# Kernel tuning notes

Hardware: AMD Instinct MI355X
Metric: run time of the kernel (lower is better)

Reference implementation:

```python
import jax, jax.numpy as jnp
import numpy as np

D, H, F, Z = 768, 12, 2048, 100   # d_model, nhead, dim_feedforward, d_z
NL = 2                            # num enc layers == num dec layers
RATIO = 0.05                      # filter_ratio
EPS = 1e-5


def _ln(x, g, b):
    m = x.mean(-1, keepdims=True)
    v = ((x - m) ** 2).mean(-1, keepdims=True)
    return (x - m) / jnp.sqrt(v + EPS) * g + b


def _mha(x, bias, qkv_w, qkv_b, out_w, out_b):
    # x: [N, L, D] (torch seq-first: seq=N responses, batch=L token positions)
    # bias: [L, N] float key-padding mask, ADDED to logits (torch float-mask semantics)
    N, L, _ = x.shape
    hd = D // H
    qkv = jnp.einsum('nld,ed->nle', x, qkv_w) + qkv_b
    q, k, v = jnp.split(qkv, 3, axis=-1)
    q = q.reshape(N, L, H, hd)
    k = k.reshape(N, L, H, hd)
    v = v.reshape(N, L, H, hd)
    scores = jnp.einsum('nlhd,mlhd->lhnm', q, k) / jnp.sqrt(jnp.float32(hd))
    scores = scores + bias[:, None, None, :]
    attn = jax.nn.softmax(scores, axis=-1)
    o = jnp.einsum('lhnm,mlhd->nlhd', attn, v).reshape(N, L, D)
    return o @ out_w.T + out_b


def _stack(x, bias, p):
    qkv_w, qkv_b, out_w, out_b, g1, b1, w1, c1, w2, c2, g2, b2 = p
    for i in range(NL):  # post-norm TransformerEncoderLayer, relu FFN, eval (no dropout)
        a = _mha(x, bias, qkv_w[i], qkv_b[i], out_w[i], out_b[i])
        x = _ln(x + a, g1[i], b1[i])
        f = jax.nn.relu(x @ w1[i].T + c1[i]) @ w2[i].T + c2[i]
        x = _ln(x + f, g2[i], b2[i])
    return x


def _anomaly_scores(emb, msk, enc_p, dec_p, pe_w, pe_b, pd_w, pd_b):
    bias = msk.T  # [L, N]
    h = _stack(emb, bias, enc_p)
    z = jnp.tanh(h @ pe_w.T + pe_b)
    zd = jnp.tanh(z @ pd_w.T + pd_b)
    d = _stack(zd, bias, dec_p)
    # per-response MSE between mean decoded and mean input embedding, summed over D
    return ((d.mean(axis=1) - emb.mean(axis=1)) ** 2).sum(-1)


def _forward(tree_lens, inputs_embeds, attention_mask, enc_p, dec_p, pe_w, pe_b, pd_w, pd_b):
    B, T, L, _ = inputs_embeds.shape
    tls = np.asarray(tree_lens)
    n_resp = tls - 1
    # pack ragged replies: rows 1..tree_len-1 of every tree -> [Ntot, L, D]
    b_idx = np.concatenate([np.full(n, b) for b, n in enumerate(n_resp)])
    t_idx = np.concatenate([np.arange(1, tl) for tl in tls])
    reply = inputs_embeds[b_idx, t_idx]
    masks = attention_mask[b_idx, t_idx]
    s = _anomaly_scores(reply, masks, enc_p, dec_p, pe_w, pe_b, pd_w, pd_b)  # [Ntot]
    Ntot = s.shape[0]
    # original: rank_idx = global_argsort filtered to indices < n_resp[b] (min is always 0)
    # == argsort of the FIRST n_resp[b] packed scores (faithful to the source's indexing)
    masked = jnp.where(jnp.arange(Ntot)[None, :] < jnp.asarray(n_resp)[:, None],
                       s[None, :], jnp.inf)
    order = jnp.argsort(masked, axis=1)[:, :T - 1]  # [B, T-1]
    n_ext = np.maximum(np.floor(n_resp * RATIO).astype(np.int64), 1)
    sel = np.arange(T - 1)[None, :] < n_ext[:, None]          # [B, T-1]
    selj = jnp.asarray(sel)
    node_idx = jnp.where(selj, order + 1, 0)                  # pad slots reuse src (node 0)
    node_full = jnp.concatenate([jnp.zeros((B, 1), node_idx.dtype), node_idx], axis=1)
    brow = jnp.arange(B)[:, None]
    new_emb = inputs_embeds[brow, node_full]                  # [B, T, L, D]
    valid = jnp.asarray(np.concatenate([np.ones((B, 1), bool), sel], axis=1)
                        ).astype(attention_mask.dtype)
    new_msk = attention_mask[brow, node_full] * valid[:, :, None]  # pad rows get zero mask
    ohidx = jnp.where(selj, order + 1, T)                     # dump masked scatters to col T
    oh = jnp.zeros((B, T + 1), jnp.int32).at[brow, ohidx].set(1)[:, :T].at[:, 0].set(1)
    ext_mask = jnp.repeat(oh[:, :, None], L, axis=2).reshape(B, T * L)
    new_tree_lens = jnp.asarray(1 + n_ext, dtype=jnp.int32)
    n_ext_adv = 0
    return oh, ext_mask, n_ext_adv, new_tree_lens, new_emb, new_msk


def setup_inputs() -> dict:
    B, T, L = 16, 32, 64
    key = jax.random.key(0)
    ks = list(jax.random.split(key, 4))
    inp = {
        'tree_lens': jax.random.randint(ks[0], (B,), T // 2, T + 1),
        'inputs_embeds': jax.random.normal(ks[1], (B, T, L, D), jnp.float32),
        'attention_mask': jnp.ones((B, T, L), jnp.float32),
    }
    kit = iter(jax.random.split(ks[2], 32))
    def w(shape):
        return jax.random.normal(next(kit), (NL,) + shape, jnp.float32) * 0.02
    for pre in ('enc', 'dec'):
        inp[pre + '_qkv_w'] = w((3 * D, D)); inp[pre + '_qkv_b'] = jnp.zeros((NL, 3 * D))
        inp[pre + '_out_w'] = w((D, D));     inp[pre + '_out_b'] = jnp.zeros((NL, D))
        inp[pre + '_ln1_g'] = jnp.ones((NL, D)); inp[pre + '_ln1_b'] = jnp.zeros((NL, D))
        inp[pre + '_w1'] = w((F, D)); inp[pre + '_c1'] = jnp.zeros((NL, F))
        inp[pre + '_w2'] = w((D, F)); inp[pre + '_c2'] = jnp.zeros((NL, D))
        inp[pre + '_ln2_g'] = jnp.ones((NL, D)); inp[pre + '_ln2_b'] = jnp.zeros((NL, D))
    inp['pe_w'] = jax.random.normal(next(kit), (Z, D), jnp.float32) * 0.02
    inp['pe_b'] = jnp.zeros((Z,), jnp.float32)
    inp['pd_w'] = jax.random.normal(next(kit), (D, Z), jnp.float32) * 0.02
    inp['pd_b'] = jnp.zeros((D,), jnp.float32)
    return inp


def reference(tree_lens, inputs_embeds, attention_mask,
              enc_qkv_w, enc_qkv_b, enc_out_w, enc_out_b, enc_ln1_g, enc_ln1_b,
              enc_w1, enc_c1, enc_w2, enc_c2, enc_ln2_g, enc_ln2_b,
              dec_qkv_w, dec_qkv_b, dec_out_w, dec_out_b, dec_ln1_g, dec_ln1_b,
              dec_w1, dec_c1, dec_w2, dec_c2, dec_ln2_g, dec_ln2_b,
              pe_w, pe_b, pd_w, pd_b):
    enc_p = (enc_qkv_w, enc_qkv_b, enc_out_w, enc_out_b, enc_ln1_g, enc_ln1_b,
             enc_w1, enc_c1, enc_w2, enc_c2, enc_ln2_g, enc_ln2_b)
    dec_p = (dec_qkv_w, dec_qkv_b, dec_out_w, dec_out_b, dec_ln1_g, dec_ln1_b,
             dec_w1, dec_c1, dec_w2, dec_c2, dec_ln2_g, dec_ln2_b)
    return _forward(tree_lens, inputs_embeds, attention_mask, enc_p, dec_p,
                    pe_w, pe_b, pd_w, pd_b)
```

## Files before the change

kernel.cpp:

```cpp
#include <hip/hip_runtime.h>
#include <hip/hip_bf16.h>
#include <math.h>


#define B_  16
#define T_  32
#define L_  64
#define D_  768
#define H_  12
#define F_  2048
#define ZR_ 100
#define NP_ 512
#define EPS_ 1e-5f

#define MI_NTOT  0
#define MI_NRESP 8
#define MI_OFF   32
#define MI_BIDX  64
#define MI_TIDX  576
#define MI_NODE  1088

#define WS_BIAS2 2048
#define WS_EMEAN 34816
#define WS_S     428032
#define WS_WST   428544
#define WS_BIG   1313280

#define PEB_F    (WS_WST + 196608)

#define OUT_OH   0
#define OUT_EXT  512
#define OUT_NEA  33280
#define OUT_NTL  33281
#define OUT_NEMB 33297
#define OUT_NMSK 25199121
#define OUT_XSCR 33300
#define OUT_WSTK 12616224

#define WSEG0 1769472
#define WSEG1 589824
#define WSEG2 1572864
#define WSEG3 1572864
#define WPASS 5505024

typedef __attribute__((ext_vector_type(8))) short short8;
typedef __attribute__((ext_vector_type(4))) float f32x4;

__device__ inline float bf2f(unsigned s) {
  return __uint_as_float((s & 0xffffu) << 16);
}
__device__ inline unsigned short f2bf(float x) {
  unsigned u = __float_as_uint(x);
  u += 0x7fffu + ((u >> 16) & 1u);
  return (unsigned short)(u >> 16);
}
__device__ inline unsigned pack2(float a, float b) {
  return (unsigned)f2bf(a) | ((unsigned)f2bf(b) << 16);
}

__global__ void meta_kernel(const int* __restrict__ tl, int* __restrict__ mi) {
  if (threadIdx.x != 0) return;
  int off = 0;
  for (int b = 0; b < B_; b++) {
    int nr = tl[b] - 1;
    mi[MI_NRESP + b] = nr;
    mi[MI_OFF + b] = off;
    off += nr;
  }
  mi[MI_NTOT] = off;
  for (int j = 0; j < NP_; j++) {
    int b = -1, t = 0;
    if (j < off) {
      b = 0;
      while (b + 1 < B_ && j >= mi[MI_OFF + b + 1]) b++;
      t = j - mi[MI_OFF + b] + 1;
    }
    mi[MI_BIDX + j] = b;
    mi[MI_TIDX + j] = t;
  }
}

__global__ __launch_bounds__(256) void w2bf4_kernel(
    const float* __restrict__ s0, const float* __restrict__ s1,
    const float* __restrict__ s2, const float* __restrict__ s3,
    unsigned short* __restrict__ dst) {
  const int e = blockIdx.x * 1024 + threadIdx.x * 4;
  const float* src;
  int off;
  if (e < WSEG0)                         { src = s0; off = e; }
  else if (e < WSEG0 + WSEG1)            { src = s1; off = e - WSEG0; }
  else if (e < WSEG0 + WSEG1 + WSEG2)    { src = s2; off = e - WSEG0 - WSEG1; }
  else                                   { src = s3; off = e - WSEG0 - WSEG1 - WSEG2; }
  float4 v = *(const float4*)(src + off);
  uint2 pk; pk.x = pack2(v.x, v.y); pk.y = pack2(v.z, v.w);
  *(uint2*)(dst + e) = pk;
}

__global__ __launch_bounds__(256) void pepd_stage(
    const float* __restrict__ pew, const float* __restrict__ peb,
    const float* __restrict__ pdw,
    unsigned short* __restrict__ dpe, unsigned short* __restrict__ dpd,
    float* __restrict__ dpeb) {
  const int blk = blockIdx.x, t = threadIdx.x;
  if (blk < 192) {
    const int e = blk * 1024 + t * 4;
    const int r = e / 768, c = e % 768;
    float v[4];
    #pragma unroll
    for (int j = 0; j < 4; j++) v[j] = (r < ZR_) ? pew[r * 768 + c + j] : 0.f;
    uint2 pk; pk.x = pack2(v[0], v[1]); pk.y = pack2(v[2], v[3]);
    *(uint2*)(dpe + e) = pk;
  } else if (blk < 384) {
    const int e = (blk - 192) * 1024 + t * 4;
    const int r = e / 256, c = e % 256;
    float v[4];
    #pragma unroll
    for (int j = 0; j < 4; j++) v[j] = (c + j < ZR_) ? pdw[r * ZR_ + c + j] : 0.f;
    uint2 pk; pk.x = pack2(v[0], v[1]); pk.y = pack2(v[2], v[3]);
    *(uint2*)(dpd + e) = pk;
  } else {
    dpeb[t] = (t < ZR_) ? peb[t] : 0.f;
  }
}

__global__ __launch_bounds__(192) void gather_kernel(
    const float* __restrict__ emb, const float* __restrict__ am,
    const int* __restrict__ mi, unsigned short* __restrict__ X,
    float* __restrict__ bias2) {
  const int blk = blockIdx.x;
  const int j = blk >> 6, l = blk & 63;
  const int ntot = mi[MI_NTOT];
  const int t = threadIdx.x;
  float4 v = make_float4(0.f, 0.f, 0.f, 0.f);
  if (j < ntot) {
    const int b = mi[MI_BIDX + j], tt = mi[MI_TIDX + j];
    v = ((const float4*)(emb + (size_t)((b * T_ + tt) * L_ + l) * D_))[t];
    if (t == 0) bias2[blk] = am[(b * T_ + tt) * L_ + l];
  } else {
    if (t == 0) bias2[blk] = -1e30f;
  }
  uint2 pk; pk.x = pack2(v.x, v.y); pk.y = pack2(v.z, v.w);
  *(uint2*)(X + (size_t)blk * D_ + t * 4) = pk;
}

__global__ __launch_bounds__(256) void zerotail_kernel(const int* __restrict__ mi,
                                                       unsigned short* __restrict__ BIG) {
  const int row = blockIdx.x;
  if (row < mi[MI_NTOT] * 64) return;
  uint4 z = make_uint4(0u, 0u, 0u, 0u);
  uint4* p = (uint4*)(BIG + (size_t)row * 2304);
  for (int c = threadIdx.x; c < 288; c += 256) p[c] = z;
}

__global__ __launch_bounds__(256) void emean_kernel(const unsigned short* __restrict__ X,
                                                    float* __restrict__ em) {
  const int j = blockIdx.x;
  int d = threadIdx.x;
  for (int c = 0; c < 3; c++, d += 256) {
    const unsigned short* p = X + (size_t)j * L_ * D_ + d;
    float s = 0.f;
    for (int l = 0; l < L_; l++) s += bf2f(p[l * D_]);
    em[j * D_ + d] = s * (1.f / 64.f);
  }
}

__device__ inline float blockSum256(float v, float* red) {
  #pragma unroll
  for (int o = 32; o > 0; o >>= 1) v += __shfl_down(v, o);
  const int lane = threadIdx.x & 63, wid = threadIdx.x >> 6;
  __syncthreads();
  if (lane == 0) red[wid] = v;
  __syncthreads();
  return red[0] + red[1] + red[2] + red[3];
}

__global__ __launch_bounds__(256) void ln_kernel(unsigned short* __restrict__ X,
                                                 const float* __restrict__ g,
                                                 const float* __restrict__ bb,
                                                 const int* __restrict__ mi) {
  const int row = blockIdx.x;
  if (row >= mi[MI_NTOT] * L_) return;
  unsigned short* p = X + (size_t)row * D_;
  const int t = threadIdx.x;
  __shared__ float red[4];
  float v0 = bf2f(p[t]), v1 = bf2f(p[t + 256]), v2 = bf2f(p[t + 512]);
  float s = blockSum256(v0 + v1 + v2, red);
  float m = s * (1.f / 768.f);
  float d0 = v0 - m, d1 = v1 - m, d2 = v2 - m;
  float q = blockSum256(d0 * d0 + d1 * d1 + d2 * d2, red);
  float r = rsqrtf(q * (1.f / 768.f) + EPS_);
  p[t]       = f2bf(d0 * r * g[t]       + bb[t]);
  p[t + 256] = f2bf(d1 * r * g[t + 256] + bb[t + 256]);
  p[t + 512] = f2bf(d2 * r * g[t + 512] + bb[t + 512]);
}

template <int ACT, bool ADD>
__global__ __launch_bounds__(512, 2) void gemm_mfma(
    const unsigned short* __restrict__ A, int lda, int K,
    const unsigned short* __restrict__ W, int ldw,
    const float* __restrict__ bias,
    unsigned short* __restrict__ C, int ldc, int CT,
    const int* __restrict__ mi) {
  const int rows = mi[MI_NTOT] * 64;
  const int RTa = (rows + 255) >> 8;
  const int NTa = RTa * CT;
  const int id = blockIdx.x;
  if (id >= NTa) return;
  const int q8 = NTa >> 3, r8 = NTa & 7;
  const int xcd = id & 7, idx = id >> 3;
  const int wg = (xcd < r8 ? xcd * (q8 + 1) : r8 * (q8 + 1) + (xcd - r8) * q8) + idx;
  const int row0 = (wg / CT) * 256;
  const int col0 = (wg % CT) * 256;
  __shared__ unsigned short As[2][256 * 64];
  __shared__ unsigned short Bs[2][256 * 64];
  const int t = threadIdx.x;
  const int lane = t & 63, w = t >> 6;
  const int wr = w >> 2, wc = w & 3;
  const int quad = lane >> 4, l15 = lane & 15;

  const int srow = t >> 3;
  const int sgs = (t & 7) ^ (srow & 7);
  const unsigned short* aSrc = A + (size_t)(row0 + srow) * lda + sgs * 8;
  const unsigned short* bSrc = W + (size_t)(col0 + srow) * ldw + sgs * 8;

#define STAGE_(ph, kk, Ad, Bd)                                                  \
  do {                                                                          \
    __builtin_amdgcn_global_load_lds(                                           \
        (const __attribute__((address_space(1))) void*)(aSrc + (size_t)(ph) * 64 * lda + (kk)), \
        (__attribute__((address_space(3))) void*)((Ad) + (ph) * 4096 + w * 512), 16, 0, 0); \
    __builtin_amdgcn_global_load_lds(                                           \
        (const __attribute__((address_space(1))) void*)(bSrc + (size_t)(ph) * 64 * ldw + (kk)), \
        (__attribute__((address_space(3))) void*)((Bd) + (ph) * 4096 + w * 512), 16, 0, 0); \
  } while (0)

  auto LDA_ = [&](const unsigned short* buf, int m, int ks) -> short8 {
    const int ar = wr * 128 + m * 16 + l15;
    return *(const short8*)(buf + ar * 64 + (((ks << 2) + quad) ^ (ar & 7)) * 8);
  };
  auto LDB_ = [&](const unsigned short* buf, int n, int ks) -> short8 {
    const int bn = wc * 64 + n * 16 + l15;
    return *(const short8*)(buf + bn * 64 + (((ks << 2) + quad) ^ (bn & 7)) * 8);
  };

  f32x4 acc[8][4];
  #pragma unroll
  for (int m = 0; m < 8; m++)
    #pragma unroll
    for (int n = 0; n < 4; n++) acc[m][n] = (f32x4){0.f, 0.f, 0.f, 0.f};

  STAGE_(0, 0, As[0], Bs[0]);
  STAGE_(1, 0, As[0], Bs[0]);
  STAGE_(2, 0, As[0], Bs[0]);
  STAGE_(3, 0, As[0], Bs[0]);
  __syncthreads();

  const int KT = K >> 6;
  for (int kt = 0; kt < KT; ++kt) {
    const unsigned short* Ac = As[kt & 1];
    const unsigned short* Bc = Bs[kt & 1];
    unsigned short* An = As[(kt + 1) & 1];
    unsigned short* Bn = Bs[(kt + 1) & 1];
    const int kn = (kt + 1) << 6;
    const bool more = kn < K;
    short8 afr[4], bfr[4];

    #pragma unroll
    for (int n = 0; n < 4; n++) bfr[n] = LDB_(Bc, n, 0);
    #pragma unroll
    for (int m = 0; m < 4; m++) afr[m] = LDA_(Ac, m, 0);
    if (more) STAGE_(0, kn, An, Bn);
    __builtin_amdgcn_s_setprio(1);
    #pragma unroll
    for (int m = 0; m < 4; m++)
      #pragma unroll
      for (int n = 0; n < 4; n++)
        acc[m][n] = __builtin_amdgcn_mfma_f32_16x16x32_bf16(afr[m], bfr[n], acc[m][n], 0, 0, 0);
    __builtin_amdgcn_s_setprio(0);

    #pragma unroll
    for (int m = 0; m < 4; m++) afr[m] = LDA_(Ac, m + 4, 0);
    if (more) STAGE_(1, kn, An, Bn);
    __builtin_amdgcn_s_setprio(1);
    #pragma unroll
    for (int m = 0; m < 4; m++)
      #pragma unroll
      for (int n = 0; n < 4; n++)
        acc[m + 4][n] = __builtin_amdgcn_mfma_f32_16x16x32_bf16(afr[m], bfr[n], acc[m + 4][n], 0, 0, 0);
    __builtin_amdgcn_s_setprio(0);

    #pragma unroll
    for (int n = 0; n < 4; n++) bfr[n] = LDB_(Bc, n, 1);
    #pragma unroll
    for (int m = 0; m < 4; m++) afr[m] = LDA_(Ac, m, 1);
    if (more) STAGE_(2, kn, An, Bn);
    __builtin_amdgcn_s_setprio(1);
    #pragma unroll
    for (int m = 0; m < 4; m++)
      #pragma unroll
      for (int n = 0; n < 4; n++)
        acc[m][n] = __builtin_amdgcn_mfma_f32_16x16x32_bf16(afr[m], bfr[n], acc[m][n], 0, 0, 0);
    __builtin_amdgcn_s_setprio(0);

    #pragma unroll
    for (int m = 0; m < 4; m++) afr[m] = LDA_(Ac, m + 4, 1);
    if (more) STAGE_(3, kn, An, Bn);
    __builtin_amdgcn_s_setprio(1);
    #pragma unroll
    for (int m = 0; m < 4; m++)
      #pragma unroll
      for (int n = 0; n < 4; n++)
        acc[m + 4][n] = __builtin_amdgcn_mfma_f32_16x16x32_bf16(afr[m], bfr[n], acc[m + 4][n], 0, 0, 0);
    __builtin_amdgcn_s_setprio(0);

    __syncthreads();
  }
#undef STAGE_

  float bv[4];
  #pragma unroll
  for (int n = 0; n < 4; n++) bv[n] = bias[col0 + wc * 64 + n * 16 + l15];
  #pragma unroll
  for (int m = 0; m < 8; m++) {
    #pragma unroll
    for (int reg = 0; reg < 4; reg++) {
      const size_t cr = (size_t)(row0 + wr * 128 + m * 16 + quad * 4 + reg) * ldc;
      #pragma unroll
      for (int n = 0; n < 4; n++) {
        const int cn = col0 + wc * 64 + n * 16 + l15;
        float x = acc[m][n][reg] + bv[n];
        if (ACT == 1) x = fmaxf(x, 0.f);
        if (ACT == 2) x = tanhf(x);
        if (ADD) x += bf2f(C[cr + cn]);
        C[cr + cn] = f2bf(x);
      }
    }
  }
}

__global__ __launch_bounds__(512) void attn_kernel(
    unsigned short* __restrict__ QKV, const float* __restrict__ bias2,
    const int* __restrict__ mi) {
  const int ntot = mi[MI_NTOT];
  const int lh = blockIdx.x, ntp = blockIdx.y;
  if (ntp * 128 >= ntot) return;
  const int l = lh / H_, h = lh - l * H_;
  __shared__ unsigned short QPs[128 * 64];
  __shared__ unsigned short Ks0[64 * 64], Ks1[64 * 64];
  __shared__ unsigned short Vt0[64 * 64], Vt1[64 * 64];
  __shared__ float Bls[512];
  const int t = threadIdx.x;
  const int lane = t & 63, w = t >> 6;
  const int quad = lane >> 4, l15 = lane & 15;
  const int q0 = ntp * 128;
  const size_t TSTRIDE = (size_t)64 * L_ * 2304;

  const int krow = t >> 3;
  const int kgs = (t & 7) ^ (krow & 7);
  const unsigned short* ksrc =
      QKV + (size_t)(krow * L_ + l) * 2304 + 768 + h * 64 + kgs * 8;
  const unsigned short* vsrc =
      QKV + (size_t)(lane * L_ + l) * 2304 + 1536 + h * 64 + w * 8;

  auto stageK = [&](int mt, unsigned short* Kw) {
    __builtin_amdgcn_global_load_lds(
        (const __attribute__((address_space(1))) void*)(ksrc + (size_t)mt * TSTRIDE),
        (__attribute__((address_space(3))) void*)(Kw + w * 512), 16, 0, 0);
  };
  auto scatterV = [&](uint4 a0, unsigned short* Vw) {
    const unsigned short* p0 = (const unsigned short*)&a0;
    #pragma unroll
    for (int j = 0; j < 8; j++) {
      const int d = w * 8 + j;
      Vw[d * 64 + ((lane >> 3) ^ (d & 7)) * 8 + (lane & 7)] = p0[j];
    }
  };

  #pragma unroll
  for (int r = 0; r < 2; r++) {
    const int c = r * 512 + t;
    const int row = c >> 3, g = c & 7, gs = g ^ (row & 7);
    const unsigned short* gq =
        QKV + (size_t)((q0 + row) * L_ + l) * 2304 + h * 64 + gs * 8;
    __builtin_amdgcn_global_load_lds(
        (const __attribute__((address_space(1))) void*)gq,
        (__attribute__((address_space(3))) void*)(QPs + r * 4096 + w * 512), 16, 0, 0);
  }
  stageK(0, Ks0);
  uint4 pv0 = *(const uint4*)vsrc;
  Bls[t] = bias2[t * 64 + l];
  __syncthreads();

  const int qrow = w * 16 + l15;
  short8 aq[2];
  #pragma unroll
  for (int kq = 0; kq < 2; kq++)
    aq[kq] = *(const short8*)(QPs + qrow * 64 + ((kq * 4 + quad) ^ (qrow & 7)) * 8);
  scatterV(pv0, Vt0);
  __syncthreads();

  float runmax[4], runsum[4];
  f32x4 oacc[4];
  #pragma unroll
  for (int i = 0; i < 4; i++) {
    runmax[i] = -3.0e38f; runsum[i] = 0.f;
    oacc[i] = (f32x4){0.f, 0.f, 0.f, 0.f};
  }

  auto tilecomp = [&](int mt, const unsigned short* Krd, const unsigned short* Vrd) {
    f32x4 sa[4];
    #pragma unroll
    for (int n = 0; n < 4; n++) sa[n] = (f32x4){0.f, 0.f, 0.f, 0.f};
    __builtin_amdgcn_s_setprio(1);
    #pragma unroll
    for (int n = 0; n < 4; n++) {
      const int kr = n * 16 + l15;
      #pragma unroll
      for (int kq = 0; kq < 2; kq++) {
        const short8 bk = *(const short8*)(Krd + kr * 64 + ((kq * 4 + quad) ^ (kr & 7)) * 8);
        sa[n] = __builtin_amdgcn_mfma_f32_16x16x32_bf16(aq[kq], bk, sa[n], 0, 0, 0);
      }
    }
    __builtin_amdgcn_s_setprio(0);
    float bj[4];
    #pragma unroll
    for (int n = 0; n < 4; n++) bj[n] = Bls[mt * 64 + n * 16 + l15];
    #pragma unroll
    for (int n = 0; n < 4; n++)
      #pragma unroll
      for (int reg = 0; reg < 4; reg++)
        sa[n][reg] = sa[n][reg] * 0.125f + bj[n];

    float rmax[4], psum[4];
    #pragma unroll
    for (int reg = 0; reg < 4; reg++)
      rmax[reg] = fmaxf(fmaxf(sa[0][reg], sa[1][reg]), fmaxf(sa[2][reg], sa[3][reg]));
    #pragma unroll
    for (int o = 1; o < 16; o <<= 1)
      #pragma unroll
      for (int reg = 0; reg < 4; reg++)
        rmax[reg] = fmaxf(rmax[reg], __shfl_xor(rmax[reg], o));
    #pragma unroll
    for (int reg = 0; reg < 4; reg++) {
      const float nm = fmaxf(runmax[reg], rmax[reg]);
      const float alpha = __expf(runmax[reg] - nm);
      runmax[reg] = nm;
      float s0 = 0.f;
      #pragma unroll
      for (int n = 0; n < 4; n++) {
        const float p = __expf(sa[n][reg] - nm);
        sa[n][reg] = p; s0 += p;
      }
      psum[reg] = s0;
      runsum[reg] *= alpha;
      #pragma unroll
      for (int dn = 0; dn < 4; dn++) oacc[dn][reg] *= alpha;
    }
    #pragma unroll
    for (int o = 1; o < 16; o <<= 1)
      #pragma unroll
      for (int reg = 0; reg < 4; reg++) psum[reg] += __shfl_xor(psum[reg], o);
    #pragma unroll
    for (int reg = 0; reg < 4; reg++) runsum[reg] += psum[reg];

    #pragma unroll
    for (int n = 0; n < 4; n++) {
      const int key = n * 16 + l15;
      #pragma unroll
      for (int reg = 0; reg < 4; reg++) {
        const int qr = w * 16 + quad * 4 + reg;
        QPs[qr * 64 + ((key >> 3) ^ (qr & 7)) * 8 + (key & 7)] = f2bf(sa[n][reg]);
      }
    }
    short8 ap[2];
    #pragma unroll
    for (int kq = 0; kq < 2; kq++)
      ap[kq] = *(const short8*)(QPs + qrow * 64 + ((kq * 4 + quad) ^ (qrow & 7)) * 8);

    __builtin_amdgcn_s_setprio(1);
    #pragma unroll
    for (int dn = 0; dn < 4; dn++) {
      const int dr = dn * 16 + l15;
      #pragma unroll
      for (int kq = 0; kq < 2; kq++) {
        const short8 bv = *(const short8*)(Vrd + dr * 64 + ((kq * 4 + quad) ^ (dr & 7)) * 8);
        oacc[dn] = __builtin_amdgcn_mfma_f32_16x16x32_bf16(ap[kq], bv, oacc[dn], 0, 0, 0);
      }
    }
    __builtin_amdgcn_s_setprio(0);
  };

  for (int mt2 = 0; mt2 < 8; mt2 += 2) {
    {
      stageK(mt2 + 1, Ks1);
      uint4 n0 = *(const uint4*)(vsrc + (size_t)(mt2 + 1) * TSTRIDE);
      tilecomp(mt2, Ks0, Vt0);
      scatterV(n0, Vt1);
      __syncthreads();
    }
    {
      const bool more = (mt2 + 2) < 8;
      uint4 m0 = make_uint4(0, 0, 0, 0);
      if (more) {
        stageK(mt2 + 2, Ks0);
        m0 = *(const uint4*)(vsrc + (size_t)(mt2 + 2) * TSTRIDE);
      }
      tilecomp(mt2 + 1, Ks1, Vt1);
      if (more) scatterV(m0, Vt0);
      __syncthreads();
    }
  }

  #pragma unroll
  for (int reg = 0; reg < 4; reg++) {
    const float inv = 1.f / runsum[reg];
    const int q = q0 + w * 16 + quad * 4 + reg;
    unsigned short* op = QKV + (size_t)(q * L_ + l) * 2304 + h * 64;
    #pragma unroll
    for (int dn = 0; dn < 4; dn++)
      op[dn * 16 + l15] = f2bf(oacc[dn][reg] * inv);
  }
}

__global__ __launch_bounds__(256) void score_kernel(const unsigned short* __restrict__ X,
                                                    const float* __restrict__ em,
                                                    float* __restrict__ Sv) {
  const int j = blockIdx.x;
  const int t = threadIdx.x;
  __shared__ float red[4];
  float part = 0.f;
  for (int c = 0; c < 3; c++) {
    const int d = t + c * 256;
    const unsigned short* p = X + (size_t)j * L_ * D_ + d;
    float s = 0.f;
    for (int l = 0; l < L_; l++) s += bf2f(p[l * D_]);
    const float diff = s * (1.f / 64.f) - em[j * D_ + d];
    part += diff * diff;
  }
  const float tot = blockSum256(part, red);
  if (t == 0) Sv[j] = tot;
}

__global__ __launch_bounds__(256) void finalize_kernel(const float* __restrict__ Sv,
                                                       int* __restrict__ mi,
                                                       float* __restrict__ out) {
  const int t = threadIdx.x;
  if (t < B_) {
    const int nr = mi[MI_NRESP + t];
    float best = 3.0e38f; int bi = 0;
    for (int j = 0; j < nr; j++) {
      const float v = Sv[j];
      if (v < best) { best = v; bi = j; }
    }
    mi[MI_NODE + t] = bi + 1;
    int next = nr / 20; if (next < 1) next = 1;
    out[OUT_NTL + t] = (float)(1 + next);
  }
  if (t == 0) out[OUT_NEA] = 0.f;
  __syncthreads();
  for (int idx = t; idx < B_ * T_; idx += 256) {
    const int b = idx >> 5, tt = idx & 31;
    out[OUT_OH + idx] = (tt == 0 || tt == mi[MI_NODE + b]) ? 1.f : 0.f;
  }
}

__global__ __launch_bounds__(256) void maskout_kernel(const float* __restrict__ am,
                                                      const int* __restrict__ mi,
                                                      float* __restrict__ out) {
  const int idx = blockIdx.x * 256 + threadIdx.x;
  const int b = idx >> 11, rem = idx & 2047;
  const int tt = rem >> 6, l = rem & 63;
  const int node = mi[MI_NODE + b];
  out[OUT_EXT + idx] = (tt == 0 || tt == node) ? 1.f : 0.f;
  float nm;
  if (tt == 0)      nm = am[(b * T_) * L_ + l];
  else if (tt == 1) nm = am[(b * T_ + node) * L_ + l];
  else              nm = 0.f;
  out[OUT_NMSK + idx] = nm;
}

__global__ __launch_bounds__(192) void newemb_kernel(const float* __restrict__ emb,
                                                     const int* __restrict__ mi,
                                                     float* __restrict__ out) {
  const int blk = blockIdx.x;
  const int b = blk >> 11, rem = blk & 2047;
  const int tt = rem >> 6, l = rem & 63;
  const int srct = (tt == 1) ? mi[MI_NODE + b] : 0;
  const float4 v = ((const float4*)(emb + (size_t)((b * T_ + srct) * L_ + l) * D_))[threadIdx.x];
  float* dst = out + OUT_NEMB + (size_t)blk * D_ + threadIdx.x * 4;
  dst[0] = v.x; dst[1] = v.y; dst[2] = v.z; dst[3] = v.w;
}

extern "C" void kernel_launch(void* const* d_in, const int* in_sizes, int n_in,
                              void* d_out, int out_size, void* d_ws, size_t ws_size,
                              hipStream_t stream) {
  (void)in_sizes; (void)n_in; (void)out_size; (void)ws_size;
  const int*   tl  = (const int*)d_in[0];
  const float* emb = (const float*)d_in[1];
  const float* am  = (const float*)d_in[2];
  const float* P[28];
  for (int i = 0; i < 28; i++) P[i] = (const float*)d_in[3 + i];

  float* wsf   = (float*)d_ws;
  int*   mi    = (int*)d_ws;
  float* bias2 = wsf + WS_BIAS2;
  float* emean = wsf + WS_EMEAN;
  float* Sv    = wsf + WS_S;
  unsigned short* Wst = (unsigned short*)(wsf + WS_WST);
  unsigned short* peW = Wst;
  unsigned short* pdW = Wst + 196608;
  float* peB   = wsf + PEB_F;
  unsigned short* BIG = (unsigned short*)(wsf + WS_BIG);
  unsigned short* Zs  = (unsigned short*)(wsf + WS_BIG);
  float* out   = (float*)d_out;
  unsigned short* X    = (unsigned short*)(out + OUT_XSCR);
  unsigned short* WSTK = (unsigned short*)(out + OUT_WSTK);

  meta_kernel<<<1, 64, 0, stream>>>(tl, mi);
  for (int p = 0; p < 4; p++) {
    const float* const* q = P + (p >> 1) * 12;
    const int i = p & 1;
    w2bf4_kernel<<<WPASS / 1024, 256, 0, stream>>>(
        q[0] + (size_t)i * 3 * D_ * D_, q[2] + (size_t)i * D_ * D_,
        q[6] + (size_t)i * F_ * D_, q[8] + (size_t)i * D_ * F_,
        WSTK + (size_t)p * WPASS);
  }
  pepd_stage<<<385, 256, 0, stream>>>(P[24], P[25], P[26], peW, pdW, peB);
  gather_kernel<<<NP_ * L_, 192, 0, stream>>>(emb, am, mi, X, bias2);
  emean_kernel<<<NP_, 256, 0, stream>>>(X, emean);
  zerotail_kernel<<<NP_ * L_, 256, 0, stream>>>(mi, BIG);

  const int RT2 = NP_ * 64 / 256;
  for (int s = 0; s < 2; s++) {
    const float* const* q = P + s * 12;
    for (int i = 0; i < 2; i++) {
      const unsigned short* WP = WSTK + (size_t)(s * 2 + i) * WPASS;
      gemm_mfma<0, false><<<RT2 * 9, 512, 0, stream>>>(
          X, D_, D_, WP, D_, q[1] + i * 3 * D_, BIG, 3 * D_, 9, mi);
      attn_kernel<<<dim3(L_ * H_, 4), 512, 0, stream>>>(BIG, bias2, mi);
      gemm_mfma<0, true><<<RT2 * 3, 512, 0, stream>>>(
          BIG, 3 * D_, D_, WP + WSEG0, D_, q[3] + i * D_, X, D_, 3, mi);
      ln_kernel<<<NP_ * L_, 256, 0, stream>>>(X, q[4] + i * D_, q[5] + i * D_, mi);
      gemm_mfma<1, false><<<RT2 * 8, 512, 0, stream>>>(
          X, D_, D_, WP + WSEG0 + WSEG1, D_, q[7] + i * F_, BIG, F_, 8, mi);
      gemm_mfma<0, true><<<RT2 * 3, 512, 0, stream>>>(
          BIG, F_, F_, WP + WSEG0 + WSEG1 + WSEG2, F_, q[9] + i * D_, X, D_, 3, mi);
      ln_kernel<<<NP_ * L_, 256, 0, stream>>>(X, q[10] + i * D_, q[11] + i * D_, mi);
    }
    if (s == 0) {
      gemm_mfma<2, false><<<RT2 * 1, 512, 0, stream>>>(
          X, D_, D_, peW, D_, peB, Zs, 256, 1, mi);
      gemm_mfma<2, false><<<RT2 * 3, 512, 0, stream>>>(
          Zs, 256, 256, pdW, 256, P[27], X, D_, 3, mi);
    }
  }

  score_kernel<<<NP_, 256, 0, stream>>>(X, emean, Sv);
  finalize_kernel<<<1, 256, 0, stream>>>(Sv, mi, out);
  maskout_kernel<<<128, 256, 0, stream>>>(am, mi, out);
  newemb_kernel<<<B_ * T_ * L_, 192, 0, stream>>>(emb, mi, out);
}
```

Measured before the change: 2.844 ms.

## Halve GEMM K-tile, transpose attention score MFMA, remap attention blocks per XCD

The GEMM K tile drops from 64 to 32, halving LDS use per block (64KB vs 128KB) so more blocks can be resident, and the swizzle and staging are adapted to match. The cost is twice as many loop iterations and barriers. The attention kernel computes scores transposed (K as A operand), so each lane holds one query row. This cuts softmax row reductions to two cross-lane shuffles and lets bias load as a float4. Attention blocks also move to a 1D grid remapped so consecutive (l,h) pairs spread across XCDs.

```diff
diff --git a/kernel.cpp b/kernel.cpp
--- a/kernel.cpp
+++ b/kernel.cpp
@@ -211,35 +211,35 @@
   const int wg = (xcd < r8 ? xcd * (q8 + 1) : r8 * (q8 + 1) + (xcd - r8) * q8) + idx;
   const int row0 = (wg / CT) * 256;
   const int col0 = (wg % CT) * 256;
-  __shared__ unsigned short As[2][256 * 64];
-  __shared__ unsigned short Bs[2][256 * 64];
+  __shared__ unsigned short As[2][256 * 32];
+  __shared__ unsigned short Bs[2][256 * 32];
   const int t = threadIdx.x;
   const int lane = t & 63, w = t >> 6;
   const int wr = w >> 2, wc = w & 3;
   const int quad = lane >> 4, l15 = lane & 15;
 
-  const int srow = t >> 3;
-  const int sgs = (t & 7) ^ (srow & 7);
+  const int srow = t >> 2;
+  const int sgs = (t & 3) ^ ((srow >> 1) & 3);
   const unsigned short* aSrc = A + (size_t)(row0 + srow) * lda + sgs * 8;
   const unsigned short* bSrc = W + (size_t)(col0 + srow) * ldw + sgs * 8;
 
 #define STAGE_(ph, kk, Ad, Bd)                                                  \
   do {                                                                          \
     __builtin_amdgcn_global_load_lds(                                           \
-        (const __attribute__((address_space(1))) void*)(aSrc + (size_t)(ph) * 64 * lda + (kk)), \
+        (const __attribute__((address_space(1))) void*)(aSrc + (size_t)(ph) * 128 * lda + (kk)), \
         (__attribute__((address_space(3))) void*)((Ad) + (ph) * 4096 + w * 512), 16, 0, 0); \
     __builtin_amdgcn_global_load_lds(                                           \
-        (const __attribute__((address_space(1))) void*)(bSrc + (size_t)(ph) * 64 * ldw + (kk)), \
+        (const __attribute__((address_space(1))) void*)(bSrc + (size_t)(ph) * 128 * ldw + (kk)), \
         (__attribute__((address_space(3))) void*)((Bd) + (ph) * 4096 + w * 512), 16, 0, 0); \
   } while (0)
 
-  auto LDA_ = [&](const unsigned short* buf, int m, int ks) -> short8 {
+  auto LDA_ = [&](const unsigned short* buf, int m) -> short8 {
     const int ar = wr * 128 + m * 16 + l15;
-    return *(const short8*)(buf + ar * 64 + (((ks << 2) + quad) ^ (ar & 7)) * 8);
+    return *(const short8*)(buf + ar * 32 + (quad ^ ((ar >> 1) & 3)) * 8);
   };
-  auto LDB_ = [&](const unsigned short* buf, int n, int ks) -> short8 {
+  auto LDB_ = [&](const unsigned short* buf, int n) -> short8 {
     const int bn = wc * 64 + n * 16 + l15;
-    return *(const short8*)(buf + bn * 64 + (((ks << 2) + quad) ^ (bn & 7)) * 8);
+    return *(const short8*)(buf + bn * 32 + (quad ^ ((bn >> 1) & 3)) * 8);
   };
 
   f32x4 acc[8][4];
@@ -250,24 +250,22 @@
 
   STAGE_(0, 0, As[0], Bs[0]);
   STAGE_(1, 0, As[0], Bs[0]);
-  STAGE_(2, 0, As[0], Bs[0]);
-  STAGE_(3, 0, As[0], Bs[0]);
   __syncthreads();
 
-  const int KT = K >> 6;
+  const int KT = K >> 5;
   for (int kt = 0; kt < KT; ++kt) {
     const unsigned short* Ac = As[kt & 1];
     const unsigned short* Bc = Bs[kt & 1];
     unsigned short* An = As[(kt + 1) & 1];
     unsigned short* Bn = Bs[(kt + 1) & 1];
-    const int kn = (kt + 1) << 6;
+    const int kn = (kt + 1) << 5;
     const bool more = kn < K;
     short8 afr[4], bfr[4];
 
     #pragma unroll
-    for (int n = 0; n < 4; n++) bfr[n] = LDB_(Bc, n, 0);
-    #pragma unroll
-    for (int m = 0; m < 4; m++) afr[m] = LDA_(Ac, m, 0);
+    for (int n = 0; n < 4; n++) bfr[n] = LDB_(Bc, n);
+    #pragma unroll
+    for (int m = 0; m < 4; m++) afr[m] = LDA_(Ac, m);
     if (more) STAGE_(0, kn, An, Bn);
     __builtin_amdgcn_s_setprio(1);
     #pragma unroll
@@ -278,32 +276,8 @@
     __builtin_amdgcn_s_setprio(0);
 
     #pragma unroll
-    for (int m = 0; m < 4; m++) afr[m] = LDA_(Ac, m + 4, 0);
+    for (int m = 0; m < 4; m++) afr[m] = LDA_(Ac, m + 4);
     if (more) STAGE_(1, kn, An, Bn);
-    __builtin_amdgcn_s_setprio(1);
-    #pragma unroll
-    for (int m = 0; m < 4; m++)
-      #pragma unroll
-      for (int n = 0; n < 4; n++)
-        acc[m + 4][n] = __builtin_amdgcn_mfma_f32_16x16x32_bf16(afr[m], bfr[n], acc[m + 4][n], 0, 0, 0);
-    __builtin_amdgcn_s_setprio(0);
-
-    #pragma unroll
-    for (int n = 0; n < 4; n++) bfr[n] = LDB_(Bc, n, 1);
-    #pragma unroll
-    for (int m = 0; m < 4; m++) afr[m] = LDA_(Ac, m, 1);
-    if (more) STAGE_(2, kn, An, Bn);
-    __builtin_amdgcn_s_setprio(1);
-    #pragma unroll
-    for (int m = 0; m < 4; m++)
-      #pragma unroll
-      for (int n = 0; n < 4; n++)
-        acc[m][n] = __builtin_amdgcn_mfma_f32_16x16x32_bf16(afr[m], bfr[n], acc[m][n], 0, 0, 0);
-    __builtin_amdgcn_s_setprio(0);
-
-    #pragma unroll
-    for (int m = 0; m < 4; m++) afr[m] = LDA_(Ac, m + 4, 1);
-    if (more) STAGE_(3, kn, An, Bn);
     __builtin_amdgcn_s_setprio(1);
     #pragma unroll
     for (int m = 0; m < 4; m++)
@@ -341,8 +315,11 @@
     unsigned short* __restrict__ QKV, const float* __restrict__ bias2,
     const int* __restrict__ mi) {
   const int ntot = mi[MI_NTOT];
-  const int lh = blockIdx.x, ntp = blockIdx.y;
+  const int id = blockIdx.x;
+  const int xcd = id & 7, rr = id >> 3;
+  const int ntp = rr & 3, lhi = rr >> 2;
   if (ntp * 128 >= ntot) return;
+  const int lh = lhi * 8 + xcd;
   const int l = lh / H_, h = lh - l * H_;
   __shared__ unsigned short QPs[128 * 64];
   __shared__ unsigned short Ks0[64 * 64], Ks1[64 * 64];
@@ -398,13 +375,10 @@
   scatterV(pv0, Vt0);
   __syncthreads();
 
-  float runmax[4], runsum[4];
+  float runmax = -3.0e38f, runsum = 0.f;
   f32x4 oacc[4];
   #pragma unroll
-  for (int i = 0; i < 4; i++) {
-    runmax[i] = -3.0e38f; runsum[i] = 0.f;
-    oacc[i] = (f32x4){0.f, 0.f, 0.f, 0.f};
-  }
+  for (int i = 0; i < 4; i++) oacc[i] = (f32x4){0.f, 0.f, 0.f, 0.f};
 
   auto tilecomp = [&](int mt, const unsigned short* Krd, const unsigned short* Vrd) {
     f32x4 sa[4];
@@ -417,60 +391,55 @@
       #pragma unroll
       for (int kq = 0; kq < 2; kq++) {
         const short8 bk = *(const short8*)(Krd + kr * 64 + ((kq * 4 + quad) ^ (kr & 7)) * 8);
-        sa[n] = __builtin_amdgcn_mfma_f32_16x16x32_bf16(aq[kq], bk, sa[n], 0, 0, 0);
+        sa[n] = __builtin_amdgcn_mfma_f32_16x16x32_bf16(bk, aq[kq], sa[n], 0, 0, 0);
       }
     }
     __builtin_amdgcn_s_setprio(0);
-    float bj[4];
-    #pragma unroll
-    for (int n = 0; n < 4; n++) bj[n] = Bls[mt * 64 + n * 16 + l15];
+    #pragma unroll
+    for (int n = 0; n < 4; n++) {
+      const float4 bj = *(const float4*)(Bls + mt * 64 + n * 16 + quad * 4);
+      sa[n][0] = sa[n][0] * 0.125f + bj.x;
+      sa[n][1] = sa[n][1] * 0.125f + bj.y;
+      sa[n][2] = sa[n][2] * 0.125f + bj.z;
+      sa[n][3] = sa[n][3] * 0.125f + bj.w;
+    }
+
+    float m16 = -3.0e38f;
     #pragma unroll
     for (int n = 0; n < 4; n++)
-      #pragma unroll
-      for (int reg = 0; reg < 4; reg++)
-        sa[n][reg] = sa[n][reg] * 0.125f + bj[n];
-
-    float rmax[4], psum[4];
+      m16 = fmaxf(m16, fmaxf(fmaxf(sa[n][0], sa[n][1]), fmaxf(sa[n][2], sa[n][3])));
+    m16 = fmaxf(m16, __shfl_xor(m16, 16));
+    m16 = fmaxf(m16, __shfl_xor(m16, 32));
+    const float nm = fmaxf(runmax, m16);
+    const float alpha = __expf(runmax - nm);
+    runmax = nm;
+    float s16 = 0.f;
+    #pragma unroll
+    for (int n = 0; n < 4; n++)
+      #pragma unroll
+      for (int reg = 0; reg < 4; reg++) {
+        const float p = __expf(sa[n][reg] - nm);
+        sa[n][reg] = p; s16 += p;
+      }
+    s16 += __shfl_xor(s16, 16);
+    s16 += __shfl_xor(s16, 32);
+    runsum = runsum * alpha + s16;
+    float al[4];
     #pragma unroll
     for (int reg = 0; reg < 4; reg++)
-      rmax[reg] = fmaxf(fmaxf(sa[0][reg], sa[1][reg]), fmaxf(sa[2][reg], sa[3][reg]));
-    #pragma unroll
-    for (int o = 1; o < 16; o <<= 1)
-      #pragma unroll
-      for (int reg = 0; reg < 4; reg++)
-        rmax[reg] = fmaxf(rmax[reg], __shfl_xor(rmax[reg], o));
-    #pragma unroll
-    for (int reg = 0; reg < 4; reg++) {
-      const float nm = fmaxf(runmax[reg], rmax[reg]);
-      const float alpha = __expf(runmax[reg] - nm);
-      runmax[reg] = nm;
-      float s0 = 0.f;
-      #pragma unroll
-      for (int n = 0; n < 4; n++) {
-        const float p = __expf(sa[n][reg] - nm);
-        sa[n][reg] = p; s0 += p;
+      al[reg] = __shfl(alpha, (lane & 48) | (quad * 4 + reg));
+    #pragma unroll
+    for (int dn = 0; dn < 4; dn++)
+      #pragma unroll
+      for (int reg = 0; reg < 4; reg++) oacc[dn][reg] *= al[reg];
+
+    #pragma unroll
+    for (int n = 0; n < 4; n++)
+      #pragma unroll
+      for (int reg = 0; reg < 4; reg++) {
+        const int key = n * 16 + quad * 4 + reg;
+        QPs[qrow * 64 + ((key >> 3) ^ (qrow & 7)) * 8 + (key & 7)] = f2bf(sa[n][reg]);
       }
-      psum[reg] = s0;
-      runsum[reg] *= alpha;
-      #pragma unroll
-      for (int dn = 0; dn < 4; dn++) oacc[dn][reg] *= alpha;
-    }
-    #pragma unroll
-    for (int o = 1; o < 16; o <<= 1)
-      #pragma unroll
-      for (int reg = 0; reg < 4; reg++) psum[reg] += __shfl_xor(psum[reg], o);
-    #pragma unroll
-    for (int reg = 0; reg < 4; reg++) runsum[reg] += psum[reg];
-
-    #pragma unroll
-    for (int n = 0; n < 4; n++) {
-      const int key = n * 16 + l15;
-      #pragma unroll
-      for (int reg = 0; reg < 4; reg++) {
-        const int qr = w * 16 + quad * 4 + reg;
-        QPs[qr * 64 + ((key >> 3) ^ (qr & 7)) * 8 + (key & 7)] = f2bf(sa[n][reg]);
-      }
-    }
     short8 ap[2];
     #pragma unroll
     for (int kq = 0; kq < 2; kq++)
@@ -510,14 +479,18 @@
     }
   }
 
+  const float inv = 1.f / runsum;
+  float iv[4];
+  #pragma unroll
+  for (int reg = 0; reg < 4; reg++)
+    iv[reg] = __shfl(inv, (lane & 48) | (quad * 4 + reg));
   #pragma unroll
   for (int reg = 0; reg < 4; reg++) {
-    const float inv = 1.f / runsum[reg];
     const int q = q0 + w * 16 + quad * 4 + reg;
     unsigned short* op = QKV + (size_t)(q * L_ + l) * 2304 + h * 64;
     #pragma unroll
     for (int dn = 0; dn < 4; dn++)
-      op[dn * 16 + l15] = f2bf(oacc[dn][reg] * inv);
+      op[dn * 16 + l15] = f2bf(oacc[dn][reg] * iv[reg]);
   }
 }
 
@@ -636,7 +609,7 @@
       const unsigned short* WP = WSTK + (size_t)(s * 2 + i) * WPASS;
       gemm_mfma<0, false><<<RT2 * 9, 512, 0, stream>>>(
           X, D_, D_, WP, D_, q[1] + i * 3 * D_, BIG, 3 * D_, 9, mi);
-      attn_kernel<<<dim3(L_ * H_, 4), 512, 0, stream>>>(BIG, bias2, mi);
+      attn_kernel<<<L_ * H_ * 4, 512, 0, stream>>>(BIG, bias2, mi);
       gemm_mfma<0, true><<<RT2 * 3, 512, 0, stream>>>(
           BIG, 3 * D_, D_, WP + WSEG0, D_, q[3] + i * D_, X, D_, 3, mi);
       ln_kernel<<<NP_ * L_, 256, 0, stream>>>(X, q[4] + i * D_, q[5] + i * D_, mi);
```

Result: no change. 2.867 ms (+0.8%).
